# Kernel tuning notes

Measured on AMD Instinct MI355X. Metric: run time of the kernel, lower is better.

Reference implementation:

```python
import jax, jax.numpy as jnp
import numpy as np

DIM = 128
HEADS = 4
HD = DIM // HEADS  # 32
WS = 8             # search window (ws x ws candidates)
K = 16             # top-k neighbors kept
SCALE = HD ** -0.5


def _sepconv(x, w_dw, w_pw, b):
    # depthwise 3x3 ('SAME', reflect-free) + pointwise 1x1 with bias (SepConv2d)
    C = x.shape[1]
    y = jax.lax.conv_general_dilated(x, w_dw, (1, 1), 'SAME',
                                     feature_group_count=C,
                                     dimension_numbers=('NCHW', 'OIHW', 'NCHW'))
    return jnp.einsum('bchw,oc->bohw', y, w_pw) + b[None, :, None, None]


def _refl(i, n):
    # dnls reflect_bounds: mirror indices back into [0, n-1]
    i = jnp.where(i < 0, -i, i)
    return jnp.where(i >= n, 2 * (n - 1) - i, i)


def _neighbor_idx(T, H, W, ws):
    # flat pixel index of the ws*ws spatial candidates per query (wt=0: same frame)
    off = jnp.arange(ws) - ws // 2
    ni = _refl(jnp.arange(H)[:, None] + off[None, :], H)  # [H,ws]
    nj = _refl(jnp.arange(W)[:, None] + off[None, :], W)  # [W,ws]
    pix = ni[:, None, :, None] * W + nj[None, :, None, :]  # [H,W,ws,ws]
    idx = jnp.arange(T)[:, None, None, None, None] * (H * W) + pix[None]
    return idx.reshape(T * H * W, ws * ws).astype(jnp.int32)  # [Q,L]


def reference(vid, wq_dw, wq_pw, bq, wk_dw, wk_pw, bk, wv_dw, wv_pw, bv, proj_w, proj_b):
    B, T, C, H, W = vid.shape
    Q = T * H * W
    x = vid.reshape(B * T, C, H, W)
    # qkv conv projection; q pre-scaled as in get_qkv
    q = _sepconv(x, wq_dw, wq_pw, bq) * SCALE
    k = _sepconv(x, wk_dw, wk_pw, bk)
    v = _sepconv(x, wv_dw, wv_pw, bv)

    def heads(z):  # [B*T,C,H,W] -> [B,heads,Q,hd]
        return z.reshape(B, T, HEADS, HD, H, W).transpose(0, 2, 1, 4, 5, 3).reshape(B, HEADS, Q, HD)

    qh, kh, vh = heads(q), heads(k), heads(v)
    idx = _neighbor_idx(T, H, W, WS)            # [Q,L]
    kg = jnp.take(kh, idx, axis=2)              # [B,h,Q,L,hd] irregular gather
    dists = jnp.einsum('bhqd,bhqld->bhql', qh, kg)
    vals, args = jax.lax.top_k(dists, K)        # k-NN by prod distance
    attn = jax.nn.softmax(vals, axis=-1)        # run_softmax over k
    sel = jnp.take_along_axis(jnp.broadcast_to(idx[None, None], (B, HEADS) + idx.shape), args, axis=-1)
    vsel = jnp.take_along_axis(vh, sel.reshape(B, HEADS, Q * K)[..., None], axis=2).reshape(B, HEADS, Q, K, HD)
    out = jnp.einsum('bhqk,bhqkd->bhqd', attn, vsel)   # wpsum (ps=pt=1)
    out = out.transpose(0, 2, 1, 3).reshape(B, Q, C)   # merge heads: (h c)
    y = out @ proj_w.T + proj_b                        # nn.Linear proj
    # fold: ps=1, stride0=1 -> zvid==1, pure reshape back to video
    return y.reshape(B, T, H, W, C).transpose(0, 1, 4, 2, 3)


def setup_inputs() -> dict:
    key = jax.random.key(0)
    ks = jax.random.split(key, 12)
    s = 0.02
    return {
        'vid': jax.random.normal(ks[0], (1, 2, DIM, 96, 96), jnp.float32),
        'wq_dw': jax.random.normal(ks[1], (DIM, 1, 3, 3), jnp.float32) * s,
        'wq_pw': jax.random.normal(ks[2], (DIM, DIM), jnp.float32) * s,
        'bq': jax.random.normal(ks[3], (DIM,), jnp.float32) * s,
        'wk_dw': jax.random.normal(ks[4], (DIM, 1, 3, 3), jnp.float32) * s,
        'wk_pw': jax.random.normal(ks[5], (DIM, DIM), jnp.float32) * s,
        'bk': jax.random.normal(ks[6], (DIM,), jnp.float32) * s,
        'wv_dw': jax.random.normal(ks[7], (DIM, 1, 3, 3), jnp.float32) * s,
        'wv_pw': jax.random.normal(ks[8], (DIM, DIM), jnp.float32) * s,
        'bv': jax.random.normal(ks[9], (DIM,), jnp.float32) * s,
        'proj_w': jax.random.normal(ks[10], (DIM, DIM), jnp.float32) * s,
        'proj_b': jax.random.normal(ks[11], (DIM,), jnp.float32) * s,
    }
```

## Files before the change

### kernel.cpp

```cpp
#include <hip/hip_runtime.h>
#include <math.h>

#define TT 2
#define CH 128
#define HH 96
#define WW 96
#define HWS 9216
#define QTOT 18432
#define QC (QTOT*CH)
#define HD 32
#define KTOP 16
#define SCALE 0.17677669529663687f

#define SEG 16
#define PR 8
#define PC 23
#define PSTRIDE 36

#define WB_TOT 98304

typedef __attribute__((ext_vector_type(8))) short short8;
typedef __attribute__((ext_vector_type(4))) float floatx4;

__device__ __forceinline__ unsigned short f2bf(float f) {
    union { float f; unsigned u; } x; x.f = f;
    unsigned r = x.u + 0x7fffu + ((x.u >> 16) & 1u);
    return (unsigned short)(r >> 16);
}
__device__ __forceinline__ float bf2f(unsigned short h) {
    return __uint_as_float(((unsigned)h) << 16);
}

__device__ __forceinline__ int refl(int x, int n) {
    x = x < 0 ? -x : x;
    return x >= n ? 2 * (n - 1) - x : x;
}

__global__ __launch_bounds__(256) void dwcvt_kernel(
    const float* __restrict__ x,
    const float* __restrict__ wq, const float* __restrict__ wk, const float* __restrict__ wv,
    const float* __restrict__ wq_pw, const float* __restrict__ wk_pw,
    const float* __restrict__ wv_pw, const float* __restrict__ proj_w,
    unsigned short* __restrict__ qk_hi,
    unsigned short* __restrict__ qk_lo,
    unsigned short* __restrict__ v_bf,
    unsigned short* __restrict__ wbuf)
{
    int t = threadIdx.x;
    if (blockIdx.x == 288) {
        int y = blockIdx.y;
        const float* src = y == 0 ? wq_pw : (y == 1 ? wk_pw : (y == 2 ? wv_pw : proj_w));
        unsigned short* hi = wbuf + (y == 0 ? 0 : (y == 1 ? 32768 : (y == 2 ? 65536 : 81920)));
#pragma unroll
        for (int r = 0; r < 16; r++) {
            int idx = r * 256 + t;
            float4 w4 = *(const float4*)(src + idx * 4);
            unsigned short hx = f2bf(w4.x), hy = f2bf(w4.y), hz = f2bf(w4.z), hw = f2bf(w4.w);
            uint2 pk;
            pk.x = hx | ((unsigned)hy << 16); pk.y = hz | ((unsigned)hw << 16);
            *(uint2*)(hi + idx * 4) = pk;
            if (y < 2) {
                unsigned short lx = f2bf(w4.x - bf2f(hx)), ly = f2bf(w4.y - bf2f(hy));
                unsigned short lz = f2bf(w4.z - bf2f(hz)), lw = f2bf(w4.w - bf2f(hw));
                pk.x = lx | ((unsigned)ly << 16); pk.y = lz | ((unsigned)lw << 16);
                *(uint2*)(hi + 16384 + idx * 4) = pk;
            }
        }
        return;
    }

    int pl = t & 63;
    int cg = __builtin_amdgcn_readfirstlane(t >> 6);
    int p  = blockIdx.x * 64 + pl;
    int c0 = blockIdx.y * 32 + cg * 8;
    int hw = p % HWS;
    int tt = p / HWS;
    int i = hw / WW, j = hw % WW;

    unsigned qh[4], ql[4], kh[4], kl[4], vh4[4];
#pragma unroll
    for (int ic = 0; ic < 8; ic += 2) {
        float sv[3][2];
#pragma unroll
        for (int u = 0; u < 2; u++) {
            int c = c0 + ic + u;
            const float* xp = x + (size_t)(tt * CH + c) * HWS;
            float w0[9], w1[9], w2[9];
#pragma unroll
            for (int r = 0; r < 9; r++) {
                w0[r] = wq[c * 9 + r]; w1[r] = wk[c * 9 + r]; w2[r] = wv[c * 9 + r];
            }
            float s0 = 0.f, s1 = 0.f, s2 = 0.f;
#pragma unroll
            for (int r = 0; r < 3; r++) {
                int ii = i + r - 1;
                if (ii < 0 || ii >= HH) continue;
#pragma unroll
                for (int ss = 0; ss < 3; ss++) {
                    int jj = j + ss - 1;
                    if (jj < 0 || jj >= WW) continue;
                    float xv = xp[ii * WW + jj];
                    s0 += xv * w0[r * 3 + ss];
                    s1 += xv * w1[r * 3 + ss];
                    s2 += xv * w2[r * 3 + ss];
                }
            }
            sv[0][u] = s0; sv[1][u] = s1; sv[2][u] = s2;
        }
        int w = ic >> 1;
        unsigned short h0 = f2bf(sv[0][0]), h1 = f2bf(sv[0][1]);
        qh[w] = h0 | ((unsigned)h1 << 16);
        ql[w] = f2bf(sv[0][0] - bf2f(h0)) | ((unsigned)f2bf(sv[0][1] - bf2f(h1)) << 16);
        h0 = f2bf(sv[1][0]); h1 = f2bf(sv[1][1]);
        kh[w] = h0 | ((unsigned)h1 << 16);
        kl[w] = f2bf(sv[1][0] - bf2f(h0)) | ((unsigned)f2bf(sv[1][1] - bf2f(h1)) << 16);
        vh4[w] = f2bf(sv[2][0]) | ((unsigned)f2bf(sv[2][1]) << 16);
    }
    size_t off = (size_t)p * CH + c0;
    uint4 pk;
    pk.x = qh[0]; pk.y = qh[1]; pk.z = qh[2]; pk.w = qh[3];
    *(uint4*)(qk_hi + off) = pk;
    pk.x = ql[0]; pk.y = ql[1]; pk.z = ql[2]; pk.w = ql[3];
    *(uint4*)(qk_lo + off) = pk;
    pk.x = kh[0]; pk.y = kh[1]; pk.z = kh[2]; pk.w = kh[3];
    *(uint4*)(qk_hi + (size_t)QC + off) = pk;
    pk.x = kl[0]; pk.y = kl[1]; pk.z = kl[2]; pk.w = kl[3];
    *(uint4*)(qk_lo + (size_t)QC + off) = pk;
    pk.x = vh4[0]; pk.y = vh4[1]; pk.z = vh4[2]; pk.w = vh4[3];
    *(uint4*)(v_bf + off) = pk;
}

__global__ __launch_bounds__(256) void qkv_mfma(
    const unsigned short* __restrict__ Ahi,
    const unsigned short* __restrict__ Alo,
    const unsigned short* __restrict__ Avb,
    const unsigned short* __restrict__ wbuf,
    const float* __restrict__ bq, const float* __restrict__ bk, const float* __restrict__ bv,
    float* __restrict__ qkf,
    unsigned short* __restrict__ vh)
{
    __shared__ unsigned short WhS[128 * 136];
    __shared__ unsigned short WlS[128 * 136];
    int sel = blockIdx.y;
    int t = threadIdx.x;
    int wv = t >> 6, lane = t & 63;
    int m = lane & 15, quad = lane >> 4;
    int p0 = blockIdx.x * 64;
    int o0 = wv * 32;

    if (sel == 2) {
        const unsigned short* Wg = wbuf + 65536;
#pragma unroll
        for (int r = 0; r < 16; r++) {
            int lin = r * 256 + t;
            int o = lin >> 5, cq = lin & 31;
            *(uint2*)(&WhS[o * 136 + cq * 4]) = *(const uint2*)(Wg + o * CH + cq * 4);
        }
        __syncthreads();
        float bb[2];
#pragma unroll
        for (int ot = 0; ot < 2; ot++) bb[ot] = bv[o0 + ot * 16 + m];
        floatx4 acc[4][2];
#pragma unroll
        for (int i = 0; i < 4; i++)
#pragma unroll
            for (int j = 0; j < 2; j++) acc[i][j] = (floatx4){0.f, 0.f, 0.f, 0.f};
#pragma unroll
        for (int kc = 0; kc < 4; kc++) {
            short8 a[4], b[2];
#pragma unroll
            for (int pt = 0; pt < 4; pt++)
                a[pt] = *(const short8*)(Avb + (size_t)(p0 + pt * 16 + m) * CH + kc * 32 + quad * 8);
#pragma unroll
            for (int ot = 0; ot < 2; ot++)
                b[ot] = *(const short8*)(&WhS[(o0 + ot * 16 + m) * 136 + kc * 32 + quad * 8]);
#pragma unroll
            for (int pt = 0; pt < 4; pt++)
#pragma unroll
                for (int ot = 0; ot < 2; ot++)
                    acc[pt][ot] = __builtin_amdgcn_mfma_f32_16x16x32_bf16(a[pt], b[ot], acc[pt][ot], 0, 0, 0);
        }
        unsigned short* vhh = vh + (size_t)wv * QTOT * 32;
#pragma unroll
        for (int pt = 0; pt < 4; pt++)
#pragma unroll
            for (int ot = 0; ot < 2; ot++)
#pragma unroll
                for (int reg = 0; reg < 4; reg++) {
                    int p = p0 + pt * 16 + quad * 4 + reg;
                    vhh[(size_t)p * 32 + ot * 16 + m] = f2bf(acc[pt][ot][reg] + bb[ot]);
                }
        return;
    }

    const unsigned short* Wh_g = wbuf + sel * 32768;
    const unsigned short* Wl_g = Wh_g + 16384;
    const float* bias = sel ? bk : bq;
    float scale = sel ? 1.f : SCALE;
    const unsigned short* ah = Ahi + (size_t)sel * QC;
    const unsigned short* al = Alo + (size_t)sel * QC;
    float* O = qkf + (size_t)sel * QC;

#pragma unroll
    for (int r = 0; r < 16; r++) {
        int lin = r * 256 + t;
        int o = lin >> 5, cq = lin & 31;
        *(uint2*)(&WhS[o * 136 + cq * 4]) = *(const uint2*)(Wh_g + o * CH + cq * 4);
        *(uint2*)(&WlS[o * 136 + cq * 4]) = *(const uint2*)(Wl_g + o * CH + cq * 4);
    }
    __syncthreads();
    float bb[2];
#pragma unroll
    for (int ot = 0; ot < 2; ot++) bb[ot] = bias[o0 + ot * 16 + m];
    floatx4 acc[4][2];
#pragma unroll
    for (int i = 0; i < 4; i++)
#pragma unroll
        for (int j = 0; j < 2; j++) acc[i][j] = (floatx4){0.f, 0.f, 0.f, 0.f};
#pragma unroll
    for (int kc = 0; kc < 4; kc++) {
        short8 avh[4], avl[4], bh[2], bl[2];
#pragma unroll
        for (int pt = 0; pt < 4; pt++) {
            size_t base = (size_t)(p0 + pt * 16 + m) * CH + kc * 32 + quad * 8;
            avh[pt] = *(const short8*)(ah + base);
            avl[pt] = *(const short8*)(al + base);
        }
#pragma unroll
        for (int ot = 0; ot < 2; ot++) {
            int lidx = (o0 + ot * 16 + m) * 136 + kc * 32 + quad * 8;
            bh[ot] = *(const short8*)(&WhS[lidx]);
            bl[ot] = *(const short8*)(&WlS[lidx]);
        }
#pragma unroll
        for (int pt = 0; pt < 4; pt++)
#pragma unroll
            for (int ot = 0; ot < 2; ot++) {
                acc[pt][ot] = __builtin_amdgcn_mfma_f32_16x16x32_bf16(avh[pt], bh[ot], acc[pt][ot], 0, 0, 0);
                acc[pt][ot] = __builtin_amdgcn_mfma_f32_16x16x32_bf16(avh[pt], bl[ot], acc[pt][ot], 0, 0, 0);
                acc[pt][ot] = __builtin_amdgcn_mfma_f32_16x16x32_bf16(avl[pt], bh[ot], acc[pt][ot], 0, 0, 0);
            }
    }
#pragma unroll
    for (int pt = 0; pt < 4; pt++)
#pragma unroll
        for (int ot = 0; ot < 2; ot++)
#pragma unroll
            for (int reg = 0; reg < 4; reg++) {
                int p = p0 + pt * 16 + quad * 4 + reg;
                O[(size_t)p * CH + o0 + ot * 16 + m] = (acc[pt][ot][reg] + bb[ot]) * scale;
            }
}

__global__ __launch_bounds__(1024) void attn_kernel(
    const float* __restrict__ q,
    const float* __restrict__ k,
    const unsigned short* __restrict__ vh,
    unsigned short* __restrict__ att)
{
    __shared__ float kp[PR * PC * PSTRIDE];
    __shared__ uint2 slot[16][KTOP];
    int h = blockIdx.y;
    int n = blockIdx.x;
    int seg = (n & 7) * 144 + (n >> 3);
    int qj0 = (seg % (WW / SEG)) * SEG;
    int qi = (seg / (WW / SEG)) % HH;
    int tt = seg / ((WW / SEG) * HH);
    int t = threadIdx.x;

#pragma unroll
    for (int r = 0; r < 2; r++) {
        int f = r * 1024 + t;
        if (f < PR * PC * 8) {
            int pix = f >> 3, d4 = f & 7;
            int ci = pix / PC, cj = pix - ci * PC;
            int gi = refl(qi + ci - 4, HH);
            int gj = refl(qj0 + cj - 4, WW);
            int gp = tt * HWS + gi * WW + gj;
            int sw = (pix >> 3) & 7;
            *(float4*)(&kp[pix * PSTRIDE + ((d4 ^ sw) << 2)]) =
                *(const float4*)(k + (size_t)gp * CH + h * HD + d4 * 4);
        }
    }

    int wv = t >> 6, lane = t & 63;
    int wvu = __builtin_amdgcn_readfirstlane(wv);
    if (lane < KTOP) slot[wvu][lane] = make_uint2(0u, 0u);
    __syncthreads();

    int ci = lane >> 3, cjo = lane & 7;
    int di = ci - 4, dj = cjo - 4;
    int rowoff = tt * HWS + refl(qi + di, HH) * WW;
    const unsigned long long below = (1ull << lane) - 1ull;
    const unsigned short* vhh = vh + (size_t)h * QTOT * 32;

    int ql = wvu;
    int qj = qj0 + ql;
    int p = tt * HWS + qi * WW + qj;

    const float* qp = q + (size_t)p * CH + h * HD;
    int pixq = ci * PC + ql + cjo;
    const float* kr = &kp[pixq * PSTRIDE];
    int sq = (pixq >> 3) & 7;
    float dist = 0.f;
#pragma unroll
    for (int dd = 0; dd < 8; dd++) {
        float4 qv = *(const float4*)(qp + dd * 4);
        float4 kv = *(const float4*)(kr + ((dd ^ sq) << 2));
        dist += qv.x * kv.x + qv.y * kv.y + qv.z * kv.z + qv.w * kv.w;
    }

    unsigned u = __float_as_uint(dist);
    unsigned key = (u & 0x80000000u) ? ~u : (u | 0x80000000u);
    unsigned khi = key >> 16, klo = key & 0xffffu;
    float e = __expf(dist);

    unsigned Lh = 0u;
#pragma unroll
    for (int bit = 15; bit >= 0; --bit) {
        unsigned C = Lh | (1u << bit);
        unsigned long long b = __ballot(khi >= C);
        Lh = (__popcll(b) >= KTOP) ? C : Lh;
    }
    bool gth = khi > Lh;
    bool eqh = (khi == Lh);
    unsigned long long gtmh = __ballot(gth);
    unsigned long long eqmh = __ballot(eqh);
    int need = KTOP - __popcll(gtmh);
    bool selb;
    unsigned long long selm;
    if (__popcll(eqmh) == need) {
        selb = gth || eqh;
        selm = gtmh | eqmh;
    } else {
        unsigned Ll = 0u;
#pragma unroll
        for (int bit = 15; bit >= 0; --bit) {
            unsigned C = Ll | (1u << bit);
            unsigned long long b = __ballot(klo >= C) & eqmh;
            Ll = (__popcll(b) >= need) ? C : Ll;
        }
        unsigned long long gtml = __ballot(klo > Ll) & eqmh;
        unsigned long long eqml = __ballot(klo == Ll) & eqmh;
        int needl = need - __popcll(gtml);
        int rk = __popcll(eqml & below);
        bool gtl = eqh && (klo > Ll);
        bool eql = eqh && (klo == Ll);
        selb = gth || gtl || (eql && rk < needl);
        selm = __ballot(selb);
    }
    int rksel = __builtin_amdgcn_mbcnt_hi(
        (unsigned)(selm >> 32), __builtin_amdgcn_mbcnt_lo((unsigned)selm, 0));
    int cpix = rowoff + refl(qj + dj, WW);
    if (selb && rksel < KTOP)
        slot[wvu][rksel] = make_uint2(__float_as_uint(e), (unsigned)(cpix << 5));

    const int d = lane & (HD - 1);
    const int half8 = (lane >> 5) * 8;
    float acc = 0.f, denom = 0.f;
#pragma unroll
    for (int r = 0; r < 8; r++) {
        uint2 sp = slot[wvu][half8 + r];
        float a0 = __uint_as_float(sp.x);
        denom += a0;
        acc += a0 * bf2f(vhh[(size_t)sp.y + d]);
    }
    acc += __shfl_xor(acc, 32);
    denom += __shfl_xor(denom, 32);
    if (lane < HD)
        att[(size_t)p * CH + h * HD + lane] =
            f2bf(acc * __builtin_amdgcn_rcpf(denom));
}

__global__ __launch_bounds__(256) void proj_mfma(
    const unsigned short* __restrict__ A,
    const unsigned short* __restrict__ wbuf,
    const float* __restrict__ bias,
    float* __restrict__ out)
{
    __shared__ unsigned short Ws[128 * 136];
    const unsigned short* Wg = wbuf + 81920;
    int t = threadIdx.x;
#pragma unroll
    for (int r = 0; r < 16; r++) {
        int lin = r * 256 + t;
        int o = lin >> 5, cq = lin & 31;
        *(uint2*)(&Ws[o * 136 + cq * 4]) = *(const uint2*)(Wg + o * CH + cq * 4);
    }
    __syncthreads();
    int wv = t >> 6, lane = t & 63;
    int m = lane & 15, quad = lane >> 4;
    int p0 = blockIdx.x * 64;
    int o0 = wv * 32;
    float bb[2][4];
#pragma unroll
    for (int ot = 0; ot < 2; ot++)
#pragma unroll
        for (int reg = 0; reg < 4; reg++) bb[ot][reg] = bias[o0 + ot * 16 + quad * 4 + reg];
    floatx4 acc[2][4];
#pragma unroll
    for (int i = 0; i < 2; i++)
#pragma unroll
        for (int j = 0; j < 4; j++) acc[i][j] = (floatx4){0.f, 0.f, 0.f, 0.f};
#pragma unroll
    for (int kc = 0; kc < 4; kc++) {
        short8 a[2], b[4];
#pragma unroll
        for (int ot = 0; ot < 2; ot++)
            a[ot] = *(const short8*)(&Ws[(o0 + ot * 16 + m) * 136 + kc * 32 + quad * 8]);
#pragma unroll
        for (int pt = 0; pt < 4; pt++)
            b[pt] = *(const short8*)(A + (size_t)(p0 + pt * 16 + m) * CH + kc * 32 + quad * 8);
#pragma unroll
        for (int ot = 0; ot < 2; ot++)
#pragma unroll
            for (int pt = 0; pt < 4; pt++)
                acc[ot][pt] = __builtin_amdgcn_mfma_f32_16x16x32_bf16(a[ot], b[pt], acc[ot][pt], 0, 0, 0);
    }
    int tt = p0 / HWS;
    int hwb = p0 - tt * HWS;
#pragma unroll
    for (int ot = 0; ot < 2; ot++)
#pragma unroll
        for (int pt = 0; pt < 4; pt++)
#pragma unroll
            for (int reg = 0; reg < 4; reg++) {
                int o = o0 + ot * 16 + quad * 4 + reg;
                int hw = hwb + pt * 16 + m;
                out[((size_t)(tt * CH + o)) * HWS + hw] = acc[ot][pt][reg] + bb[ot][reg];
            }
}

extern "C" void kernel_launch(void* const* d_in, const int* in_sizes, int n_in,
                              void* d_out, int out_size, void* d_ws, size_t ws_size,
                              hipStream_t stream) {
    const float* vid    = (const float*)d_in[0];
    const float* wq_dw  = (const float*)d_in[1];
    const float* wq_pw  = (const float*)d_in[2];
    const float* bq     = (const float*)d_in[3];
    const float* wk_dw  = (const float*)d_in[4];
    const float* wk_pw  = (const float*)d_in[5];
    const float* bk     = (const float*)d_in[6];
    const float* wv_dw  = (const float*)d_in[7];
    const float* wv_pw  = (const float*)d_in[8];
    const float* bv     = (const float*)d_in[9];
    const float* proj_w = (const float*)d_in[10];
    const float* proj_b = (const float*)d_in[11];
    float* out = (float*)d_out;

    float* qkf = (float*)d_ws;
    unsigned short* vh = (unsigned short*)(qkf + (size_t)2 * QC);
    unsigned short* qk_hi = vh + (size_t)QC;
    unsigned short* qk_lo = qk_hi + (size_t)2 * QC;
    unsigned short* v_bf = qk_lo + (size_t)2 * QC;
    unsigned short* wbuf = v_bf + (size_t)QC;
    unsigned short* att_bf = v_bf;

    dwcvt_kernel<<<dim3(289, 4), 256, 0, stream>>>(
        vid, wq_dw, wk_dw, wv_dw, wq_pw, wk_pw, wv_pw, proj_w,
        qk_hi, qk_lo, v_bf, wbuf);
    qkv_mfma<<<dim3(QTOT / 64, 3), 256, 0, stream>>>(
        qk_hi, qk_lo, v_bf, wbuf, bq, bk, bv, qkf, vh);
    attn_kernel<<<dim3(TT * HH * (WW / SEG), 4), 1024, 0, stream>>>(
        qkf, qkf + (size_t)QC, vh, att_bf);
    proj_mfma<<<QTOT / 64, 256, 0, stream>>>(att_bf, wbuf, proj_b, out);
}
```

Measured before the change: 177.6 us.

## Load GEMM weights directly from global memory and drop k-patch LDS swizzle

The qkv and projection MFMA kernels no longer stage the 128x128 weight matrices into shared memory behind a barrier. Each wave now reads its weight fragments straight from global memory, relying on L1/L2 caching. This removes per-block LDS fill and synchronisation and frees LDS for higher occupancy, but adds repeated global loads per block. Separately, the XOR swizzle on the k-patch shared-memory layout in the search kernel is removed, which simplifies indexing but may bring back LDS bank conflicts.

Result: no change. 179.4 us, median of 2 (+1.0%).

```diff
diff --git a/kernel.cpp b/kernel.cpp
--- a/kernel.cpp
+++ b/kernel.cpp
@@ -139,8 +139,6 @@
     float* __restrict__ qkf,
     unsigned short* __restrict__ vh)
 {
-    __shared__ unsigned short WhS[128 * 136];
-    __shared__ unsigned short WlS[128 * 136];
     int sel = blockIdx.y;
     int t = threadIdx.x;
     int wv = t >> 6, lane = t & 63;
@@ -150,13 +148,6 @@
 
     if (sel == 2) {
         const unsigned short* Wg = wbuf + 65536;
-#pragma unroll
-        for (int r = 0; r < 16; r++) {
-            int lin = r * 256 + t;
-            int o = lin >> 5, cq = lin & 31;
-            *(uint2*)(&WhS[o * 136 + cq * 4]) = *(const uint2*)(Wg + o * CH + cq * 4);
-        }
-        __syncthreads();
         float bb[2];
 #pragma unroll
         for (int ot = 0; ot < 2; ot++) bb[ot] = bv[o0 + ot * 16 + m];
@@ -173,7 +164,7 @@
                 a[pt] = *(const short8*)(Avb + (size_t)(p0 + pt * 16 + m) * CH + kc * 32 + quad * 8);
 #pragma unroll
             for (int ot = 0; ot < 2; ot++)
-                b[ot] = *(const short8*)(&WhS[(o0 + ot * 16 + m) * 136 + kc * 32 + quad * 8]);
+                b[ot] = *(const short8*)(Wg + (size_t)(o0 + ot * 16 + m) * CH + kc * 32 + quad * 8);
 #pragma unroll
             for (int pt = 0; pt < 4; pt++)
 #pragma unroll
@@ -201,14 +192,6 @@
     const unsigned short* al = Alo + (size_t)sel * QC;
     float* O = qkf + (size_t)sel * QC;
 
-#pragma unroll
-    for (int r = 0; r < 16; r++) {
-        int lin = r * 256 + t;
-        int o = lin >> 5, cq = lin & 31;
-        *(uint2*)(&WhS[o * 136 + cq * 4]) = *(const uint2*)(Wh_g + o * CH + cq * 4);
-        *(uint2*)(&WlS[o * 136 + cq * 4]) = *(const uint2*)(Wl_g + o * CH + cq * 4);
-    }
-    __syncthreads();
     float bb[2];
 #pragma unroll
     for (int ot = 0; ot < 2; ot++) bb[ot] = bias[o0 + ot * 16 + m];
@@ -228,9 +211,9 @@
         }
 #pragma unroll
         for (int ot = 0; ot < 2; ot++) {
-            int lidx = (o0 + ot * 16 + m) * 136 + kc * 32 + quad * 8;
-            bh[ot] = *(const short8*)(&WhS[lidx]);
-            bl[ot] = *(const short8*)(&WlS[lidx]);
+            size_t widx = (size_t)(o0 + ot * 16 + m) * CH + kc * 32 + quad * 8;
+            bh[ot] = *(const short8*)(Wh_g + widx);
+            bl[ot] = *(const short8*)(Wl_g + widx);
         }
 #pragma unroll
         for (int pt = 0; pt < 4; pt++)
@@ -277,8 +260,7 @@
             int gi = refl(qi + ci - 4, HH);
             int gj = refl(qj0 + cj - 4, WW);
             int gp = tt * HWS + gi * WW + gj;
-            int sw = (pix >> 3) & 7;
-            *(float4*)(&kp[pix * PSTRIDE + ((d4 ^ sw) << 2)]) =
+            *(float4*)(&kp[pix * PSTRIDE + d4 * 4]) =
                 *(const float4*)(k + (size_t)gp * CH + h * HD + d4 * 4);
         }
     }
@@ -301,12 +283,11 @@
     const float* qp = q + (size_t)p * CH + h * HD;
     int pixq = ci * PC + ql + cjo;
     const float* kr = &kp[pixq * PSTRIDE];
-    int sq = (pixq >> 3) & 7;
     float dist = 0.f;
 #pragma unroll
     for (int dd = 0; dd < 8; dd++) {
         float4 qv = *(const float4*)(qp + dd * 4);
-        float4 kv = *(const float4*)(kr + ((dd ^ sq) << 2));
+        float4 kv = *(const float4*)(kr + dd * 4);
         dist += qv.x * kv.x + qv.y * kv.y + qv.z * kv.z + qv.w * kv.w;
     }
 
@@ -378,16 +359,8 @@
     const float* __restrict__ bias,
     float* __restrict__ out)
 {
-    __shared__ unsigned short Ws[128 * 136];
     const unsigned short* Wg = wbuf + 81920;
     int t = threadIdx.x;
-#pragma unroll
-    for (int r = 0; r < 16; r++) {
-        int lin = r * 256 + t;
-        int o = lin >> 5, cq = lin & 31;
-        *(uint2*)(&Ws[o * 136 + cq * 4]) = *(const uint2*)(Wg + o * CH + cq * 4);
-    }
-    __syncthreads();
     int wv = t >> 6, lane = t & 63;
     int m = lane & 15, quad = lane >> 4;
     int p0 = blockIdx.x * 64;
@@ -407,7 +380,7 @@
         short8 a[2], b[4];
 #pragma unroll
         for (int ot = 0; ot < 2; ot++)
-            a[ot] = *(const short8*)(&Ws[(o0 + ot * 16 + m) * 136 + kc * 32 + quad * 8]);
+            a[ot] = *(const short8*)(Wg + (size_t)(o0 + ot * 16 + m) * CH + kc * 32 + quad * 8);
 #pragma unroll
         for (int pt = 0; pt < 4; pt++)
             b[pt] = *(const short8*)(A + (size_t)(p0 + pt * 16 + m) * CH + kc * 32 + quad * 8);
```
